# Kernel optimization log

Measured on AMD Instinct MI355X. Metric: run time of the kernel, lower is better.

The kernel has to match this reference:

```python
import jax, jax.numpy as jnp
import numpy as np

D_MODEL = 1024
NUM_HEADS = 16
NUM_KV_HEADS = 4
D_K = D_MODEL // NUM_HEADS  # 64
GROUP = NUM_HEADS // NUM_KV_HEADS  # 4
ROPE_BASE = 10000.0
NEG = -10000.0


def _rope_cos_sin(seq_len, d_k, dtype):
    # matches standard RotaryEmbedding: inv_freq over even dims, emb = cat(freqs, freqs)
    inv_freq = 1.0 / (ROPE_BASE ** (jnp.arange(0, d_k, 2, dtype=jnp.float32) / d_k))
    t = jnp.arange(seq_len, dtype=jnp.float32)
    freqs = jnp.einsum('s,f->sf', t, inv_freq)          # [S, d_k/2]
    emb = jnp.concatenate([freqs, freqs], axis=-1)       # [S, d_k]
    return jnp.cos(emb).astype(dtype), jnp.sin(emb).astype(dtype)


def _apply_rope(x, cos, sin):
    # x: [B, H, S, d_k]; cos/sin: [S, d_k] broadcast over B, H
    half = x.shape[-1] // 2
    x1, x2 = x[..., :half], x[..., half:]
    rotated = jnp.concatenate([-x2, x1], axis=-1)
    return x * cos + rotated * sin


def setup_inputs() -> dict:
    key = jax.random.key(0)
    ks = jax.random.split(key, 7)
    B, S = 2, 2048
    scale = 1.0 / np.sqrt(D_MODEL)
    return {
        'query': jax.random.normal(ks[0], (B, S, D_MODEL), dtype=jnp.float32),
        'key': jax.random.normal(ks[1], (B, S, D_MODEL), dtype=jnp.float32),
        'value': jax.random.normal(ks[2], (B, S, D_MODEL), dtype=jnp.float32),
        'Wq': jax.random.normal(ks[3], (D_MODEL, D_MODEL), dtype=jnp.float32) * scale,
        'Wk': jax.random.normal(ks[4], (NUM_KV_HEADS * D_K, D_MODEL), dtype=jnp.float32) * scale,
        'Wv': jax.random.normal(ks[5], (NUM_KV_HEADS * D_K, D_MODEL), dtype=jnp.float32) * scale,
        'Wo': jax.random.normal(ks[6], (D_MODEL, D_MODEL), dtype=jnp.float32) * scale,
    }


def reference(query, key, value, Wq, Wk, Wv, Wo):
    B, Sq, _ = query.shape
    Sk = key.shape[1]
    # projections (nn.Linear: x @ W.T)
    Q = (query @ Wq.T).reshape(B, Sq, NUM_HEADS, D_K).transpose(0, 2, 1, 3)      # [B,H,Sq,dk]
    K = (key @ Wk.T).reshape(B, Sk, NUM_KV_HEADS, D_K).transpose(0, 2, 1, 3)      # [B,Hkv,Sk,dk]
    V = (value @ Wv.T).reshape(B, Sk, NUM_KV_HEADS, D_K).transpose(0, 2, 1, 3)    # [B,Hkv,Sk,dk]
    # RoPE
    cos, sin = _rope_cos_sin(Sq, D_K, Q.dtype)
    Q = _apply_rope(Q, cos, sin)
    K = _apply_rope(K, cos[:Sk], sin[:Sk])
    # GQA attention without explicitly materializing expanded K/V:
    # group query heads as [B, Hkv, G, Sq, dk]
    Qg = Q.reshape(B, NUM_KV_HEADS, GROUP, Sq, D_K)
    scores = jnp.einsum('bhgqd,bhkd->bhgqk', Qg, K) / jnp.sqrt(jnp.float32(D_K))  # [B,Hkv,G,Sq,Sk]
    causal = jnp.tril(jnp.ones((Sq, Sk), dtype=bool))
    scores = jnp.where(causal, scores, jnp.float32(NEG))
    probs = jax.nn.softmax(scores, axis=-1)
    out = jnp.einsum('bhgqk,bhkd->bhgqd', probs, V)                                # [B,Hkv,G,Sq,dk]
    out = out.reshape(B, NUM_HEADS, Sq, D_K).transpose(0, 2, 1, 3).reshape(B, Sq, D_MODEL)
    return out @ Wo.T
```

## Files before the change

kernel.cpp:

```cpp
#include <hip/hip_runtime.h>
#include <hip/hip_bf16.h>
#include <stdint.h>

typedef __attribute__((ext_vector_type(4))) float f32x4;
typedef __attribute__((ext_vector_type(8))) short short8;

#define S_LEN 2048
#define BATCH 2
#define NH 16
#define NKV 4
#define DK 64

__device__ __forceinline__ ushort f2bf(float f) {
  __hip_bfloat16 h = __float2bfloat16(f);
  ushort u; __builtin_memcpy(&u, &h, 2); return u;
}
__device__ __forceinline__ float bf2f(ushort h) {
  union { uint32_t u; float f; } v; v.u = ((uint32_t)h) << 16;
  return v.f;
}

__device__ __forceinline__ void gld16(const void* g, void* l) {
  __builtin_amdgcn_global_load_lds((const __attribute__((address_space(1))) void*)g,
                                   (__attribute__((address_space(3))) void*)l,
                                   16, 0, 0);
}

template<int CTRL>
__device__ __forceinline__ float dpp_movf(float x) {
  return __int_as_float(__builtin_amdgcn_update_dpp(0, __float_as_int(x), CTRL, 0xF, 0xF, true));
}
__device__ __forceinline__ float rowred_sum16(float v) {
  v += dpp_movf<0xB1>(v);
  v += dpp_movf<0x4E>(v);
  v += dpp_movf<0x141>(v);
  v += dpp_movf<0x140>(v);
  return v;
}

__global__ void preproc_kernel(const float* __restrict__ w0, const float* __restrict__ w1,
                               const float* __restrict__ w2, const float* __restrict__ w3,
                               ushort* __restrict__ o0, ushort* __restrict__ o1,
                               ushort* __restrict__ o2, ushort* __restrict__ o3,
                               float* __restrict__ tab) {
  const int y = blockIdx.y, tid = threadIdx.x;
  if (y < 4) {
    int n4 = (y == 0 || y == 3) ? 262144 : 65536;
    int i = (blockIdx.x << 8) + tid;
    if (i >= n4) return;
    const float* in = y == 0 ? w0 : y == 1 ? w1 : y == 2 ? w2 : w3;
    ushort* out = y == 0 ? o0 : y == 1 ? o1 : y == 2 ? o2 : o3;
    float4 x = ((const float4*)in)[i];
    ushort4 o;
    o.x = f2bf(x.x); o.y = f2bf(x.y); o.z = f2bf(x.z); o.w = f2bf(x.w);
    ((ushort4*)out)[i] = o;
  } else {
    int j = (blockIdx.x << 8) + tid;
    if (j >= 65536) return;
    int s = j >> 5, f = j & 31;
    float freq = (float)s * powf(10000.0f, -(float)f / 32.0f);
    tab[j] = cosf(freq);
    tab[65536 + j] = sinf(freq);
  }
}

template<int EPI, int AF32>
__device__ __forceinline__ void gemm_body(const void* __restrict__ Avp,
                                          const ushort* __restrict__ W,
                                          void* __restrict__ Cout,
                                          const float* __restrict__ tab,
                                          int N, int K, int bx, int by,
                                          void* AlV, ushort* Wl) {
  const int t = threadIdx.x;
  const int lane = t & 63;
  const int w = t >> 6;
  const int wr = w >> 1, wc = w & 1;
  const int m0 = bx * 64, n0 = by * 128;
  const int g = lane >> 4, q16 = lane & 15;

  f32x4 acc[2][4] = {};

  const int lrow = lane >> 2, lcol = (lane & 3) * 8;
  const int r8 = lane >> 3, c8 = lane & 7;

  const ushort* Wp0 = W + (size_t)(n0 + w * 32 + lrow) * K + lcol;
  const ushort* Wp1 = W + (size_t)(n0 + w * 32 + 16 + lrow) * K + lcol;
  ushort* Wb0 = &Wl[(w * 32) * 32];
  ushort* Wb1 = &Wl[(w * 32 + 16) * 32];

  const ushort* Ab16 = nullptr; const float* Af32 = nullptr;
  if (AF32) Af32 = (const float*)Avp; else Ab16 = (const ushort*)Avp;

  const int KSTEPS = K >> 5;
  for (int kt = 0; kt < KSTEPS; ++kt) {
    const int k0 = kt << 5;
    __syncthreads();
    if (AF32) {
      float* Alf = (float*)AlV;
      #pragma unroll
      for (int c = 0; c < 2; ++c) {
        int row = w * 16 + c * 8 + r8;
        gld16(Af32 + (size_t)(m0 + row) * K + k0 + ((c8 ^ r8) << 2),
              Alf + (size_t)(w * 16 + c * 8) * 32);
      }
    } else {
      ushort* Alh = (ushort*)AlV;
      gld16(Ab16 + (size_t)(m0 + w * 16 + lrow) * K + k0 + lcol,
            Alh + (size_t)(w * 16) * 32);
    }
    gld16(Wp0 + k0, Wb0);
    gld16(Wp1 + k0, Wb1);
    __syncthreads();
    short8 af[2], wf[4];
    #pragma unroll
    for (int i = 0; i < 2; ++i) {
      int row = wr * 32 + i * 16 + q16;
      if (AF32) {
        const float* Alf = (const float*)AlV;
        int s0 = (g * 2) ^ (q16 & 7), s1 = (g * 2 + 1) ^ (q16 & 7);
        float4 v0 = *(const float4*)&Alf[row * 32 + s0 * 4];
        float4 v1 = *(const float4*)&Alf[row * 32 + s1 * 4];
        short8 a;
        a[0] = (short)f2bf(v0.x); a[1] = (short)f2bf(v0.y);
        a[2] = (short)f2bf(v0.z); a[3] = (short)f2bf(v0.w);
        a[4] = (short)f2bf(v1.x); a[5] = (short)f2bf(v1.y);
        a[6] = (short)f2bf(v1.z); a[7] = (short)f2bf(v1.w);
        af[i] = a;
      } else {
        const ushort* Alh = (const ushort*)AlV;
        af[i] = *(const short8*)&Alh[row * 32 + g * 8];
      }
    }
    #pragma unroll
    for (int j = 0; j < 4; ++j)
      wf[j] = *(const short8*)&Wl[(wc * 64 + j * 16 + q16) * 32 + g * 8];
    #pragma unroll
    for (int i = 0; i < 2; ++i)
      #pragma unroll
      for (int j = 0; j < 4; ++j)
        acc[i][j] = __builtin_amdgcn_mfma_f32_16x16x32_bf16(af[i], wf[j], acc[i][j], 0, 0, 0);
  }

  if (EPI == 0) {
    #pragma unroll
    for (int i = 0; i < 2; ++i)
      #pragma unroll
      for (int j = 0; j < 4; ++j) {
        int row0 = m0 + wr * 32 + i * 16 + g * 4;
        int col  = n0 + wc * 64 + j * 16 + q16;
        #pragma unroll
        for (int r = 0; r < 4; ++r)
          ((float*)Cout)[(size_t)(row0 + r) * N + col] = acc[i][j][r];
      }
  } else if (EPI == 1 || EPI == 2) {
    const int NHE = (EPI == 1) ? NH : NKV;
    const float qscale = (EPI == 1) ? 0.125f : 1.0f;
    const int h = (n0 + wc * 64) >> 6;
    ushort* O = (ushort*)Cout;
    #pragma unroll
    for (int i = 0; i < 2; ++i)
      #pragma unroll
      for (int j = 0; j < 2; ++j) {
        const int d = j * 16 + q16;
        #pragma unroll
        for (int r = 0; r < 4; ++r) {
          int row = m0 + wr * 32 + i * 16 + g * 4 + r;
          int b = row >> 11, s = row & 2047;
          float x1 = acc[i][j][r], x2 = acc[i][j + 2][r];
          float c = tab[s * 32 + d], sn = tab[65536 + s * 32 + d];
          ushort* base = O + ((size_t)(b * NHE + h) * 2048 + s) * 64;
          base[d]      = f2bf((x1 * c - x2 * sn) * qscale);
          base[d + 32] = f2bf((x2 * c + x1 * sn) * qscale);
        }
      }
  } else {
    const int h = (n0 + wc * 64) >> 6;
    ushort* O = (ushort*)Cout;
    #pragma unroll
    for (int i = 0; i < 2; ++i) {
      int row0 = m0 + wr * 32 + i * 16 + g * 4;
      int b = row0 >> 11, s0 = row0 & 2047;
      #pragma unroll
      for (int j = 0; j < 4; ++j) {
        const int d = j * 16 + q16;
        ushort4 o;
        o.x = f2bf(acc[i][j][0]); o.y = f2bf(acc[i][j][1]);
        o.z = f2bf(acc[i][j][2]); o.w = f2bf(acc[i][j][3]);
        *(ushort4*)(O + ((size_t)(b * NKV + h) * 64 + d) * 2048 + s0) = o;
      }
    }
  }
}

__global__ __launch_bounds__(256) void qkv_gemm_kernel(
    const float* __restrict__ query, const ushort* __restrict__ wqb, ushort* __restrict__ Qh,
    const float* __restrict__ key,   const ushort* __restrict__ wkb, ushort* __restrict__ Kh,
    const float* __restrict__ value, const ushort* __restrict__ wvb, ushort* __restrict__ Vt,
    const float* __restrict__ tab) {
  __shared__ float Al[64 * 32];
  __shared__ ushort Wl[128 * 32];
  const int id = blockIdx.x;
  if (id < 128) {
    gemm_body<2, 1>(key, wkb, Kh, tab, 256, 1024, id & 63, id >> 6, Al, Wl);
  } else if (id < 256) {
    const int i = id - 128;
    gemm_body<3, 1>(value, wvb, Vt, tab, 256, 1024, i & 63, i >> 6, Al, Wl);
  } else {
    const int i = id - 256;
    gemm_body<1, 1>(query, wqb, Qh, tab, 1024, 1024, i & 63, i >> 6, Al, Wl);
  }
}

__global__ __launch_bounds__(256) void o_gemm_kernel(const ushort* __restrict__ AO,
                                                     const ushort* __restrict__ wob,
                                                     float* __restrict__ out) {
  __shared__ ushort Al[64 * 32];
  __shared__ ushort Wl[128 * 32];
  gemm_body<0, 0>(AO, wob, out, nullptr, 1024, 1024, blockIdx.x & 63, blockIdx.x >> 6, Al, Wl);
}

__global__ __launch_bounds__(256) void fattn_kernel(const ushort* __restrict__ Qh,
                                                    const ushort* __restrict__ Kh,
                                                    const ushort* __restrict__ Vt,
                                                    ushort* __restrict__ AO) {
  __shared__ ushort Klds[2][4096];
  __shared__ ushort Vlds[2][4096];
  __shared__ ushort Plds[4][1024];
  const int t = threadIdx.x, lane = t & 63, wv = t >> 6;
  const int g = lane >> 4, q16 = lane & 15;

  const int hh = blockIdx.y;
  const int b = hh >> 4, h = hh & 15;
  const int kvh = h >> 2;
  const ushort* Kbase = Kh + (size_t)(b * 4 + kvh) * 2048 * 64;
  const ushort* Vbase = Vt + (size_t)(b * 4 + kvh) * 64 * 2048;

  const int r3 = lane >> 3, c3 = lane & 7;
  const int swz = (c3 ^ r3) << 3;
  const int call0 = wv * 2;

  for (int pass = 0; pass < 2; ++pass) {
    const int qt = pass ? (31 - (int)blockIdx.x) : (int)blockIdx.x;
    const int q0 = qt * 64 + wv * 16;
    const ushort* Qbase = Qh + ((size_t)hh * 2048 + q0) * 64;

    short8 aq[2];
    aq[0] = *(const short8*)(Qbase + (size_t)q16 * 64 + g * 8);
    aq[1] = *(const short8*)(Qbase + (size_t)q16 * 64 + 32 + g * 8);

    f32x4 acc[4] = {};
    float lsum[4] = {0.f, 0.f, 0.f, 0.f};

    const int nkb = qt + 1;

    __syncthreads();
    #pragma unroll
    for (int c = 0; c < 2; ++c) {
      int call = call0 + c;
      int row = call * 8 + r3;
      gld16(Kbase + (size_t)row * 64 + swz, &Klds[0][call * 512]);
      gld16(Vbase + (size_t)row * 2048 + swz, &Vlds[0][call * 512]);
    }

    int buf = 0;
    for (int kb = 0; kb < nkb; ++kb) {
      __syncthreads();
      if (kb + 1 < nkb) {
        const int k0n = (kb + 1) * 64;
        #pragma unroll
        for (int c = 0; c < 2; ++c) {
          int call = call0 + c;
          int row = call * 8 + r3;
          gld16(Kbase + (size_t)(k0n + row) * 64 + swz, &Klds[buf ^ 1][call * 512]);
          gld16(Vbase + (size_t)row * 2048 + k0n + swz, &Vlds[buf ^ 1][call * 512]);
        }
      }
      const ushort* Kl = Klds[buf];
      const ushort* Vl = Vlds[buf];
      const int k0 = kb * 64;

      f32x4 sA[4] = {};
      __builtin_amdgcn_s_setprio(1);
      #pragma unroll
      for (int kk = 0; kk < 2; ++kk)
        #pragma unroll
        for (int nt = 0; nt < 4; ++nt) {
          int row = nt * 16 + q16;
          int slot = ((kk << 2) | g) ^ (q16 & 7);
          short8 bk = *(const short8*)(Kl + row * 64 + (slot << 3));
          sA[nt] = __builtin_amdgcn_mfma_f32_16x16x32_bf16(aq[kk], bk, sA[nt], 0, 0, 0);
        }
      __builtin_amdgcn_s_setprio(0);

      if (kb == nkb - 1) {
        #pragma unroll
        for (int nt = 0; nt < 4; ++nt)
          #pragma unroll
          for (int r = 0; r < 4; ++r) {
            int col = k0 + nt * 16 + q16, row = q0 + g * 4 + r;
            if (col > row) sA[nt][r] = -1e30f;
          }
      }

      float ps[4][4];
      #pragma unroll
      for (int nt = 0; nt < 4; ++nt)
        #pragma unroll
        for (int r = 0; r < 4; ++r)
          ps[nt][r] = __expf(sA[nt][r]);
      #pragma unroll
      for (int r = 0; r < 4; ++r)
        lsum[r] += (ps[0][r] + ps[1][r]) + (ps[2][r] + ps[3][r]);

      #pragma unroll
      for (int nt = 0; nt < 4; ++nt)
        #pragma unroll
        for (int r = 0; r < 4; ++r) {
          int pr = g * 4 + r;
          Plds[wv][pr * 64 + ((nt * 16 + q16) ^ ((pr & 7) << 3))] = f2bf(ps[nt][r]);
        }
      __builtin_amdgcn_s_setprio(1);
      #pragma unroll
      for (int kk2 = 0; kk2 < 2; ++kk2) {
        int slot = ((kk2 << 2) | g) ^ (q16 & 7);
        short8 pa = *(const short8*)(&Plds[wv][q16 * 64 + (slot << 3)]);
        #pragma unroll
        for (int dt = 0; dt < 4; ++dt) {
          int rv = dt * 16 + q16;
          short8 bv = *(const short8*)(Vl + rv * 64 + (slot << 3));
          acc[dt] = __builtin_amdgcn_mfma_f32_16x16x32_bf16(pa, bv, acc[dt], 0, 0, 0);
        }
      }
      __builtin_amdgcn_s_setprio(0);

      buf ^= 1;
    }

    float linv[4];
    #pragma unroll
    for (int r = 0; r < 4; ++r) linv[r] = 1.0f / rowred_sum16(lsum[r]);
    #pragma unroll
    for (int dt = 0; dt < 4; ++dt)
      #pragma unroll
      for (int r = 0; r < 4; ++r) {
        float o = acc[dt][r] * linv[r];
        AO[((size_t)(b * 2048) + q0 + g * 4 + r) * 1024 + h * 64 + dt * 16 + q16] = f2bf(o);
      }
  }
}

extern "C" void kernel_launch(void* const* d_in, const int* in_sizes, int n_in,
                              void* d_out, int out_size, void* d_ws, size_t ws_size,
                              hipStream_t stream) {
  const float* query = (const float*)d_in[0];
  const float* key   = (const float*)d_in[1];
  const float* value = (const float*)d_in[2];
  const float* Wq    = (const float*)d_in[3];
  const float* Wk    = (const float*)d_in[4];
  const float* Wv    = (const float*)d_in[5];
  const float* Wo    = (const float*)d_in[6];
  float* out = (float*)d_out;

  char* ws = (char*)d_ws;
  size_t off = 0;
  auto alloc = [&](size_t bytes) {
    void* p = ws + off; off += (bytes + 255) & ~255ULL; return p;
  };
  ushort* wqb = (ushort*)alloc(1024ULL * 1024 * 2);
  ushort* wkb = (ushort*)alloc(256ULL * 1024 * 2);
  ushort* wvb = (ushort*)alloc(256ULL * 1024 * 2);
  ushort* wob = (ushort*)alloc(1024ULL * 1024 * 2);
  ushort* Qh  = (ushort*)alloc(4096ULL * 1024 * 2);
  ushort* Kh  = (ushort*)alloc(4096ULL * 256 * 2);
  ushort* Vt  = (ushort*)alloc(4096ULL * 256 * 2);
  ushort* AO  = (ushort*)alloc(4096ULL * 1024 * 2);
  float*  tab = (float*)alloc(2048ULL * 32 * 4 * 2);

  preproc_kernel<<<dim3(1024, 5), 256, 0, stream>>>(Wq, Wk, Wv, Wo,
                                                    wqb, wkb, wvb, wob, (float*)tab);

  qkv_gemm_kernel<<<768, 256, 0, stream>>>(query, wqb, Qh, key, wkb, Kh,
                                           value, wvb, Vt, (float*)tab);

  fattn_kernel<<<dim3(16, 32), 256, 0, stream>>>(Qh, Kh, Vt, AO);

  o_gemm_kernel<<<512, 256, 0, stream>>>(AO, wob, out);
}
```

Measured before the change: 98.83 us.

## Split attention KV range in two halves and add a combine kernel

Adds a grid z-dimension so each attention block handles only half of the causal KV blocks for its query tiles. Each half writes unnormalized fp32 accumulators and row sums to a workspace, and a new combine kernel adds the halves, normalizes, and writes the bf16 head output. The aim is to double the number of attention blocks and raise GPU occupancy and parallelism. The cost is about 32MB of extra fp32 global traffic and one more kernel launch.

```diff
diff --git a/kernel.cpp b/kernel.cpp
--- a/kernel.cpp
+++ b/kernel.cpp
@@ -222,7 +222,8 @@
 __global__ __launch_bounds__(256) void fattn_kernel(const ushort* __restrict__ Qh,
                                                     const ushort* __restrict__ Kh,
                                                     const ushort* __restrict__ Vt,
-                                                    ushort* __restrict__ AO) {
+                                                    float* __restrict__ accW,
+                                                    float* __restrict__ lsumW) {
   __shared__ ushort Klds[2][4096];
   __shared__ ushort Vlds[2][4096];
   __shared__ ushort Plds[4][1024];
@@ -230,6 +231,7 @@
   const int g = lane >> 4, q16 = lane & 15;
 
   const int hh = blockIdx.y;
+  const int hf = blockIdx.z;
   const int b = hh >> 4, h = hh & 15;
   const int kvh = h >> 2;
   const ushort* Kbase = Kh + (size_t)(b * 4 + kvh) * 2048 * 64;
@@ -252,20 +254,25 @@
     float lsum[4] = {0.f, 0.f, 0.f, 0.f};
 
     const int nkb = qt + 1;
+    const int kb_lo = hf ? (nkb >> 1) : 0;
+    const int kb_hi = hf ? nkb : (nkb >> 1);
 
     __syncthreads();
-    #pragma unroll
-    for (int c = 0; c < 2; ++c) {
-      int call = call0 + c;
-      int row = call * 8 + r3;
-      gld16(Kbase + (size_t)row * 64 + swz, &Klds[0][call * 512]);
-      gld16(Vbase + (size_t)row * 2048 + swz, &Vlds[0][call * 512]);
+    if (kb_lo < kb_hi) {
+      const int k00 = kb_lo * 64;
+      #pragma unroll
+      for (int c = 0; c < 2; ++c) {
+        int call = call0 + c;
+        int row = call * 8 + r3;
+        gld16(Kbase + (size_t)(k00 + row) * 64 + swz, &Klds[0][call * 512]);
+        gld16(Vbase + (size_t)row * 2048 + k00 + swz, &Vlds[0][call * 512]);
+      }
     }
 
     int buf = 0;
-    for (int kb = 0; kb < nkb; ++kb) {
+    for (int kb = kb_lo; kb < kb_hi; ++kb) {
       __syncthreads();
-      if (kb + 1 < nkb) {
+      if (kb + 1 < kb_hi) {
         const int k0n = (kb + 1) * 64;
         #pragma unroll
         for (int c = 0; c < 2; ++c) {
@@ -336,17 +343,39 @@
       buf ^= 1;
     }
 
-    float linv[4];
-    #pragma unroll
-    for (int r = 0; r < 4; ++r) linv[r] = 1.0f / rowred_sum16(lsum[r]);
+    float lt[4];
+    #pragma unroll
+    for (int r = 0; r < 4; ++r) lt[r] = rowred_sum16(lsum[r]);
+    const size_t rowbase = (size_t)hf * 65536 + (size_t)hh * 2048 + q0;
     #pragma unroll
     for (int dt = 0; dt < 4; ++dt)
       #pragma unroll
-      for (int r = 0; r < 4; ++r) {
-        float o = acc[dt][r] * linv[r];
-        AO[((size_t)(b * 2048) + q0 + g * 4 + r) * 1024 + h * 64 + dt * 16 + q16] = f2bf(o);
-      }
+      for (int r = 0; r < 4; ++r)
+        accW[(rowbase + g * 4 + r) * 64 + dt * 16 + q16] = acc[dt][r];
+    if (q16 == 0) {
+      #pragma unroll
+      for (int r = 0; r < 4; ++r) lsumW[rowbase + g * 4 + r] = lt[r];
+    }
   }
+}
+
+__global__ __launch_bounds__(256) void combine_kernel(const float* __restrict__ accW,
+                                                      const float* __restrict__ lsumW,
+                                                      ushort* __restrict__ AO) {
+  int i4 = blockIdx.x * 256 + threadIdx.x;
+  float4 a1 = ((const float4*)accW)[i4];
+  float4 a2 = ((const float4*)accW)[i4 + 1048576];
+  int rlin = i4 >> 4;
+  float inv = 1.0f / (lsumW[rlin] + lsumW[65536 + rlin]);
+  int d = (i4 & 15) << 2;
+  int hh = rlin >> 11, q = rlin & 2047;
+  int b = hh >> 4, h = hh & 15;
+  ushort4 o;
+  o.x = f2bf((a1.x + a2.x) * inv);
+  o.y = f2bf((a1.y + a2.y) * inv);
+  o.z = f2bf((a1.z + a2.z) * inv);
+  o.w = f2bf((a1.w + a2.w) * inv);
+  *(ushort4*)(AO + ((size_t)(b * 2048 + q) * 1024) + h * 64 + d) = o;
 }
 
 extern "C" void kernel_launch(void* const* d_in, const int* in_sizes, int n_in,
@@ -375,6 +404,8 @@
   ushort* Vt  = (ushort*)alloc(4096ULL * 256 * 2);
   ushort* AO  = (ushort*)alloc(4096ULL * 1024 * 2);
   float*  tab = (float*)alloc(2048ULL * 32 * 4 * 2);
+  float* accW = (float*)alloc(2ULL * 65536 * 64 * 4);
+  float* lsumW= (float*)alloc(2ULL * 65536 * 4);
 
   preproc_kernel<<<dim3(1024, 5), 256, 0, stream>>>(Wq, Wk, Wv, Wo,
                                                     wqb, wkb, wvb, wob, (float*)tab);
@@ -382,7 +413,9 @@
   qkv_gemm_kernel<<<768, 256, 0, stream>>>(query, wqb, Qh, key, wkb, Kh,
                                            value, wvb, Vt, (float*)tab);
 
-  fattn_kernel<<<dim3(16, 32), 256, 0, stream>>>(Qh, Kh, Vt, AO);
+  fattn_kernel<<<dim3(16, 32, 2), 256, 0, stream>>>(Qh, Kh, Vt, accW, lsumW);
+
+  combine_kernel<<<4096, 256, 0, stream>>>(accW, lsumW, AO);
 
   o_gemm_kernel<<<512, 256, 0, stream>>>(AO, wob, out);
 }
```

New measurement: 110.4 us. 11.7% more time.
